# Kernel tuning notes

Measured on AMD Instinct MI355X. Metric: run time of the kernel, lower is better.

The kernel has to match this reference:

```python
import jax, jax.numpy as jnp
import numpy as np

N_NODES = 100000
N_EDGES = 500000
B = 256
NUM_RELS = 200
VEC = 300   # rel_vectors.shape[1]
D = 32      # rel_emb_dim
MODES = 6


def setup_inputs() -> dict:
    key = jax.random.key(0)
    ks = jax.random.split(key, 16)
    s = 0.05
    return {
        'edge_src': jax.random.randint(ks[0], (N_EDGES,), 0, N_NODES, dtype=jnp.int32),
        'edge_dst': jax.random.randint(ks[1], (N_EDGES,), 0, N_NODES, dtype=jnp.int32),
        'edge_type': jax.random.randint(ks[2], (N_EDGES,), 0, NUM_RELS, dtype=jnp.int32),
        'head_ids': jnp.arange(B, dtype=jnp.int32),            # one head node per subgraph
        'tail_ids': jnp.arange(B, dtype=jnp.int32) + B,        # one tail node per subgraph (disjoint)
        'rel_labels': jax.random.randint(ks[3], (B,), 0, NUM_RELS, dtype=jnp.int32),
        'rel_vectors': jax.random.normal(ks[4], (NUM_RELS, VEC), jnp.float32),
        'W1': jax.random.normal(ks[5], (VEC, D), jnp.float32) * s,
        'b1': jax.random.normal(ks[6], (D,), jnp.float32) * s,
        'W2': jax.random.normal(ks[7], (D, D), jnp.float32) * s,
        'b2': jax.random.normal(ks[8], (D,), jnp.float32) * s,
        'reld_W': jax.random.normal(ks[9], (MODES, D, D), jnp.float32) * s,
        'reld_b': jax.random.normal(ks[10], (MODES, D), jnp.float32) * s,
        'conc_W': jax.random.normal(ks[11], (2 * D, D), jnp.float32) * s,
        'conc_b': jax.random.normal(ks[12], (D,), jnp.float32) * s,
        'fc_W': jax.random.normal(ks[13], (D, 1), jnp.float32) * s,
        'fc_b': jax.random.normal(ks[14], (1,), jnp.float32) * s,
    }


def _mode_segments(edge_src, edge_dst, head_ids, tail_ids):
    """Per-edge segment id (batch index, or B=dropped) for each of the 6 modes.
    Equivalent to the torch sparse mask build: mode5 = out_edge_out*in_edge_in,
    mode6 = in_edge_out*out_edge_in, modes 1-4 with overlaps subtracted out."""
    b = head_ids.shape[0]
    bidx = jnp.arange(b, dtype=jnp.int32)
    head_batch = jnp.full((N_NODES,), -1, jnp.int32).at[head_ids].set(bidx)
    tail_batch = jnp.full((N_NODES,), -1, jnp.int32).at[tail_ids].set(bidx)
    hb_s = head_batch[edge_src]
    hb_d = head_batch[edge_dst]
    tb_s = tail_batch[edge_src]
    tb_d = tail_batch[edge_dst]
    m5 = (hb_s >= 0) & (hb_s == tb_d)   # src==head_b and dst==tail_b
    m6 = (hb_d >= 0) & (hb_d == tb_s)   # dst==head_b and src==tail_b
    drop = jnp.int32(b)
    return [
        jnp.where((hb_d >= 0) & ~m6, hb_d, drop),  # in_edge_out  - mode6
        jnp.where((hb_s >= 0) & ~m5, hb_s, drop),  # out_edge_out - mode5
        jnp.where((tb_d >= 0) & ~m5, tb_d, drop),  # in_edge_in   - mode5
        jnp.where((tb_s >= 0) & ~m6, tb_s, drop),  # out_edge_in  - mode6
        jnp.where(m5, hb_s, drop),                 # mode5
        jnp.where(m6, hb_d, drop),                 # mode6
    ]


def reference(edge_src, edge_dst, edge_type, head_ids, tail_ids, rel_labels,
              rel_vectors, W1, b1, W2, b2, reld_W, reld_b, conc_W, conc_b, fc_W, fc_b):
    b = head_ids.shape[0]
    segs = _mode_segments(edge_src, edge_dst, head_ids, tail_ids)

    # edge embeddings: rel_vectors[type] -> transform1 -> transform2   [E, D]
    e = rel_vectors[edge_type] @ W1 + b1
    e = e @ W2 + b2
    # per-mode fc_reld transforms: [MODES, E, D]
    Y = jnp.einsum('ed,mdk->mek', e, reld_W) + reld_b[:, None, :]

    ones_e = jnp.ones(edge_src.shape, e.dtype)
    acc = jnp.zeros((b, Y.shape[-1]), e.dtype)
    for i in range(MODES):
        agg = jax.ops.segment_sum(Y[i], segs[i], num_segments=b + 1)[:b]
        cnt = jax.ops.segment_sum(ones_e, segs[i], num_segments=b + 1)[:b]
        acc = acc + agg / (cnt[:, None] + 1e-30)
    rel_neighbor = acc / MODES

    r = rel_vectors[rel_labels] @ W1 + b1
    r = r @ W2 + b2

    h = jnp.concatenate([rel_neighbor, r], axis=-1) @ conc_W + conc_b
    h = jax.nn.relu(h)
    # F.normalize(p=2, dim=-1)
    g_rep = h / jnp.maximum(jnp.linalg.norm(h, axis=-1, keepdims=True), 1e-12)
    return g_rep @ fc_W + fc_b  # [B, 1]
```

## Files before the change

kernel.cpp:

```cpp
#include <hip/hip_runtime.h>
#include <hip/hip_bf16.h>

constexpr int N_NODES  = 100000;
constexpr int BATCH    = 256;
constexpr int NUM_RELS = 200;
constexpr int VEC      = 300;
constexpr int DIM      = 32;
constexpr int MODES    = 6;

constexpr int BLOCK        = 256;
constexpr int BM_WORDS     = (N_NODES + 31) / 32;
constexpr int RELS_PER_BLK = 8;
constexpr int NRB          = NUM_RELS / RELS_PER_BLK;
static_assert(NUM_RELS % RELS_PER_BLK == 0, "rel blocks assume exact tiling");
constexpr int EDGE_BLKS    = 256;
constexpr int CAP          = 64;
constexpr int HASHN        = 1024;
constexpr unsigned HEMPTY  = 0xFFFFFFFFu;
constexpr int MAXM         = 512;

template <typename T> __device__ __forceinline__ float ldf(const void* p, int i);
template <> __device__ __forceinline__ float ldf<float>(const void* p, int i) {
    return ((const float*)p)[i];
}
template <> __device__ __forceinline__ float ldf<__hip_bfloat16>(const void* p, int i) {
    return __bfloat162float(((const __hip_bfloat16*)p)[i]);
}

__device__ __forceinline__ void detect_dtype(const void* rel_vectors, int* sflag) {
    const int tid = threadIdx.x;
    if (tid < 64) {
        unsigned short p = ((const unsigned short*)rel_vectors)[tid];
        unsigned long long mk = __ballot(((p >> 7) & 0xFF) > 140);
        if (tid == 0) *sflag = (mk == 0ull);
    }
    __syncthreads();
}

__device__ __forceinline__ void hinsert(unsigned* hkey, unsigned* hval, int node, unsigned v) {
    unsigned h = ((unsigned)node * 2654435761u) >> 22;
    for (;;) {
        unsigned prev = atomicCAS(&hkey[h], HEMPTY, (unsigned)node);
        if (prev == HEMPTY || prev == (unsigned)node) { atomicOr(&hval[h], v); return; }
        h = (h + 1) & (HASHN - 1);
    }
}
__device__ __forceinline__ unsigned hlookup(const unsigned* hkey, const unsigned* hval, int node) {
    unsigned h = ((unsigned)node * 2654435761u) >> 22;
    for (;;) {
        const unsigned k = hkey[h];
        if (k == (unsigned)node) return hval[h];
        if (k == HEMPTY) return 0u;
        h = (h + 1) & (HASHN - 1);
    }
}

template <typename T>
__device__ __forceinline__ void rel_body(const void* rel_vectors, const void* W1, const void* b1,
                                         const void* W2, const void* b2,
                                         const void* reld_W, const void* reld_b,
                                         float* E_rel, float* Y_rel,
                                         float (*rv)[VEC], float (*e1)[DIM], float (*e2)[DIM],
                                         int r0) {
    const int tid = threadIdx.x;
    const int g = tid >> 5, d = tid & 31;
    const int r = r0 + g;
    for (int v = d; v < VEC; v += 32) rv[g][v] = ldf<T>(rel_vectors, r * VEC + v);
    __syncthreads();
    float acc = ldf<T>(b1, d);
    for (int v = 0; v < VEC; ++v) acc += rv[g][v] * ldf<T>(W1, v * DIM + d);
    e1[g][d] = acc;
    __syncthreads();
    float a2 = ldf<T>(b2, d);
    for (int k = 0; k < DIM; ++k) a2 += e1[g][k] * ldf<T>(W2, k * DIM + d);
    e2[g][d] = a2;
    E_rel[r * DIM + d] = a2;
    __syncthreads();
    for (int m = 0; m < MODES; ++m) {
        float y = ldf<T>(reld_b, m * DIM + d);
        for (int k = 0; k < DIM; ++k) y += e2[g][k] * ldf<T>(reld_W, (m * DIM + k) * DIM + d);
        Y_rel[(m * NUM_RELS + r) * DIM + d] = y;
    }
}

struct EdgeSmem {
    unsigned bm[BM_WORDS];
    unsigned hkey[HASHN];
    unsigned hval[HASHN];
    unsigned obuf[CAP];
    int ocnt;
};
struct RelSmem {
    float rv[RELS_PER_BLK][VEC];
    float e1[RELS_PER_BLK][DIM];
    float e2[RELS_PER_BLK][DIM];
    int sflag;
};

__global__ __launch_bounds__(BLOCK) void k_main(
        const int* __restrict__ edge_src, const int* __restrict__ edge_dst,
        const int* __restrict__ edge_type,
        const int* __restrict__ head_ids, const int* __restrict__ tail_ids,
        const void* rel_vectors, const void* W1, const void* b1,
        const void* W2, const void* b2, const void* reld_W, const void* reld_b,
        unsigned* list, unsigned* listcnt, float* E_rel, float* Y_rel, int n_edges) {
    union SmemU { RelSmem rel; EdgeSmem edge; };
    __shared__ SmemU s;
    const int bid = blockIdx.x, tid = threadIdx.x;

    if (bid < NRB) {
        detect_dtype(rel_vectors, &s.rel.sflag);
        const int r0 = bid * RELS_PER_BLK;
        if (s.rel.sflag)
            rel_body<__hip_bfloat16>(rel_vectors, W1, b1, W2, b2, reld_W, reld_b,
                                     E_rel, Y_rel, s.rel.rv, s.rel.e1, s.rel.e2, r0);
        else
            rel_body<float>(rel_vectors, W1, b1, W2, b2, reld_W, reld_b,
                            E_rel, Y_rel, s.rel.rv, s.rel.e1, s.rel.e2, r0);
        return;
    }

    const int eb = bid - NRB;
    for (int i = tid; i < BM_WORDS; i += BLOCK) s.edge.bm[i] = 0u;
    for (int i = tid; i < HASHN; i += BLOCK) { s.edge.hkey[i] = HEMPTY; s.edge.hval[i] = 0u; }
    if (tid == 0) s.edge.ocnt = 0;
    __syncthreads();
    if (tid < BATCH) {
        const int h = head_ids[tid], t = tail_ids[tid];
        atomicOr(&s.edge.bm[h >> 5], 1u << (h & 31));
        atomicOr(&s.edge.bm[t >> 5], 1u << (t & 31));
        hinsert(s.edge.hkey, s.edge.hval, h, (unsigned)(tid + 1));
        hinsert(s.edge.hkey, s.edge.hval, t, (unsigned)(tid + 1) << 16);
    }
    __syncthreads();

    auto emit = [&](unsigned code) {
        const int idx = atomicAdd(&s.edge.ocnt, 1);
        if (idx < CAP) s.edge.obuf[idx] = code;
    };
    auto classify = [&](int sn, int dn, unsigned bs, unsigned bd, int e) {
        const int t = edge_type[e];
        const unsigned ps = bs ? hlookup(s.edge.hkey, s.edge.hval, sn) : 0u;
        const unsigned pd = bd ? hlookup(s.edge.hkey, s.edge.hval, dn) : 0u;
        const int hbs = (int)(ps & 0xFFFFu) - 1, tbs = (int)(ps >> 16) - 1;
        const int hbd = (int)(pd & 0xFFFFu) - 1, tbd = (int)(pd >> 16) - 1;
        const bool m5 = (hbs >= 0) && (hbs == tbd);
        const bool m6 = (hbd >= 0) && (hbd == tbs);
        if (hbd >= 0)        emit(((m6 ? 5u : 0u) * BATCH + hbd) * NUM_RELS + t);
        if (hbs >= 0)        emit(((m5 ? 4u : 1u) * BATCH + hbs) * NUM_RELS + t);
        if (tbd >= 0 && !m5) emit((2u * BATCH + tbd) * NUM_RELS + t);
        if (tbs >= 0 && !m6) emit((3u * BATCH + tbs) * NUM_RELS + t);
    };

    const int n4 = n_edges >> 2;
    const int sstr = EDGE_BLKS * BLOCK;
    const int et = eb * BLOCK + tid;
    const int4* src4 = (const int4*)edge_src;
    const int4* dst4 = (const int4*)edge_dst;
    for (int i = et; i < n4; i += sstr) {
        const int4 s4 = src4[i];
        const int4 d4 = dst4[i];
        #pragma unroll
        for (int j = 0; j < 4; ++j) {
            const int sn = (&s4.x)[j];
            const int dn = (&d4.x)[j];
            const unsigned bs = (s.edge.bm[sn >> 5] >> (sn & 31)) & 1u;
            const unsigned bd = (s.edge.bm[dn >> 5] >> (dn & 31)) & 1u;
            if (!(bs | bd)) continue;
            classify(sn, dn, bs, bd, i * 4 + j);
        }
    }
    const int rem = n_edges & 3;
    if (et < rem) {
        const int e = n4 * 4 + et;
        const int sn = edge_src[e], dn = edge_dst[e];
        const unsigned bs = (s.edge.bm[sn >> 5] >> (sn & 31)) & 1u;
        const unsigned bd = (s.edge.bm[dn >> 5] >> (dn & 31)) & 1u;
        if (bs | bd) classify(sn, dn, bs, bd, e);
    }
    __syncthreads();
    const int oc = min(s.edge.ocnt, CAP);
    if (tid == 0) listcnt[eb] = (unsigned)oc;
    for (int i = tid; i < oc; i += BLOCK) list[i * EDGE_BLKS + eb] = s.edge.obuf[i];
}

template <typename T>
__device__ __forceinline__ void epilogue_math(const float* cat,
                                              const void* conc_W, const void* conc_b,
                                              const void* fc_W, const void* fc_b,
                                              void* out, int b) {
    const int tid = threadIdx.x;
    if (tid < DIM) {
        float h = ldf<T>(conc_b, tid);
        for (int k = 0; k < 2 * DIM; ++k) h += cat[k] * ldf<T>(conc_W, k * DIM + tid);
        h = fmaxf(h, 0.f);
        float n2 = h * h;
        #pragma unroll
        for (int off = 16; off >= 1; off >>= 1) n2 += __shfl_xor(n2, off);
        const float g = h / fmaxf(sqrtf(n2), 1e-12f);
        float pr = g * ldf<T>(fc_W, tid);
        #pragma unroll
        for (int off = 16; off >= 1; off >>= 1) pr += __shfl_xor(pr, off);
        if (tid == 0) {
            const float o = pr + ldf<T>(fc_b, 0);
            if constexpr (sizeof(T) == 2) ((__hip_bfloat16*)out)[b] = __float2bfloat16(o);
            else                          ((float*)out)[b] = o;
        }
    }
}

__global__ __launch_bounds__(256) void k_final(
        const unsigned* __restrict__ list, const unsigned* __restrict__ listcnt,
        const float* __restrict__ E_rel, const float* __restrict__ Y_rel,
        const int* __restrict__ rel_labels, const void* rel_vectors,
        const void* conc_W, const void* conc_b, const void* fc_W, const void* fc_b,
        void* out) {
    __shared__ float    accf[MODES][DIM];
    __shared__ float    totf[MODES];
    __shared__ unsigned mbuf[MAXM];
    __shared__ int      mcnt;
    __shared__ float    cat[2 * DIM];
    __shared__ int      sflag;
    const int b = blockIdx.x, tid = threadIdx.x;

    for (int i = tid; i < MODES * DIM; i += 256) ((float*)accf)[i] = 0.f;
    if (tid < MODES) totf[tid] = 0.f;
    if (tid == 0) mcnt = 0;
    const int c = (int)listcnt[tid];
    detect_dtype(rel_vectors, &sflag);

    for (int i = 0; i < c; ++i) {
        const unsigned code = list[i * EDGE_BLKS + tid];
        const int bb = (int)((code / NUM_RELS) % BATCH);
        if (bb == b) {
            const int k = atomicAdd(&mcnt, 1);
            if (k < MAXM) mbuf[k] = code;
        }
    }
    __syncthreads();

    const int mc = min(mcnt, MAXM);
    const int d = tid & 31;
    for (int j = tid >> 5; j < mc; j += 8) {
        const unsigned code = mbuf[j];
        const int m = (int)(code / (NUM_RELS * BATCH));
        const int t = (int)(code % NUM_RELS);
        atomicAdd(&accf[m][d], Y_rel[(m * NUM_RELS + t) * DIM + d]);
        if (d == 0) atomicAdd(&totf[m], 1.f);
    }
    __syncthreads();

    if (tid < DIM) {
        float rn = 0.f;
        for (int m = 0; m < MODES; ++m) rn += accf[m][tid] / (totf[m] + 1e-30f);
        cat[tid] = rn / (float)MODES;
        cat[DIM + tid] = E_rel[rel_labels[b] * DIM + tid];
    }
    __syncthreads();
    if (sflag) epilogue_math<__hip_bfloat16>(cat, conc_W, conc_b, fc_W, fc_b, out, b);
    else       epilogue_math<float>(cat, conc_W, conc_b, fc_W, fc_b, out, b);
}

extern "C" void kernel_launch(void* const* d_in, const int* in_sizes, int n_in,
                              void* d_out, int out_size, void* d_ws, size_t ws_size,
                              hipStream_t stream) {
    const int* edge_src   = (const int*)d_in[0];
    const int* edge_dst   = (const int*)d_in[1];
    const int* edge_type  = (const int*)d_in[2];
    const int* head_ids   = (const int*)d_in[3];
    const int* tail_ids   = (const int*)d_in[4];
    const int* rel_labels = (const int*)d_in[5];
    const void* rel_vectors = d_in[6];
    const void* W1     = d_in[7];
    const void* b1     = d_in[8];
    const void* W2     = d_in[9];
    const void* b2     = d_in[10];
    const void* reld_W = d_in[11];
    const void* reld_b = d_in[12];
    const void* conc_W = d_in[13];
    const void* conc_b = d_in[14];
    const void* fc_W   = d_in[15];
    const void* fc_b   = d_in[16];

    const int n_edges = in_sizes[0];

    unsigned* list    = (unsigned*)d_ws;
    unsigned* listcnt = list + EDGE_BLKS * CAP;
    float*    E_rel   = (float*)(listcnt + EDGE_BLKS);
    float*    Y_rel   = E_rel + NUM_RELS * DIM;

    k_main<<<NRB + EDGE_BLKS, BLOCK, 0, stream>>>(
        edge_src, edge_dst, edge_type, head_ids, tail_ids,
        rel_vectors, W1, b1, W2, b2, reld_W, reld_b,
        list, listcnt, E_rel, Y_rel, n_edges);
    k_final<<<BATCH, 256, 0, stream>>>(
        list, listcnt, E_rel, Y_rel, rel_labels, rel_vectors,
        conc_W, conc_b, fc_W, fc_b, d_out);
}
```

Measured before the change: 116.3 us.

## Fuse main and final kernels with a grid-wide atomic barrier

```diff
diff --git a/kernel.cpp b/kernel.cpp
--- a/kernel.cpp
+++ b/kernel.cpp
@@ -18,6 +18,7 @@
 constexpr int HASHN        = 1024;
 constexpr unsigned HEMPTY  = 0xFFFFFFFFu;
 constexpr int MAXM         = 512;
+constexpr int NPROD        = NRB + EDGE_BLKS;
 
 template <typename T> __device__ __forceinline__ float ldf(const void* p, int i);
 template <> __device__ __forceinline__ float ldf<float>(const void* p, int i) {
@@ -81,107 +82,6 @@
         for (int k = 0; k < DIM; ++k) y += e2[g][k] * ldf<T>(reld_W, (m * DIM + k) * DIM + d);
         Y_rel[(m * NUM_RELS + r) * DIM + d] = y;
     }
-}
-
-struct EdgeSmem {
-    unsigned bm[BM_WORDS];
-    unsigned hkey[HASHN];
-    unsigned hval[HASHN];
-    unsigned obuf[CAP];
-    int ocnt;
-};
-struct RelSmem {
-    float rv[RELS_PER_BLK][VEC];
-    float e1[RELS_PER_BLK][DIM];
-    float e2[RELS_PER_BLK][DIM];
-    int sflag;
-};
-
-__global__ __launch_bounds__(BLOCK) void k_main(
-        const int* __restrict__ edge_src, const int* __restrict__ edge_dst,
-        const int* __restrict__ edge_type,
-        const int* __restrict__ head_ids, const int* __restrict__ tail_ids,
-        const void* rel_vectors, const void* W1, const void* b1,
-        const void* W2, const void* b2, const void* reld_W, const void* reld_b,
-        unsigned* list, unsigned* listcnt, float* E_rel, float* Y_rel, int n_edges) {
-    union SmemU { RelSmem rel; EdgeSmem edge; };
-    __shared__ SmemU s;
-    const int bid = blockIdx.x, tid = threadIdx.x;
-
-    if (bid < NRB) {
-        detect_dtype(rel_vectors, &s.rel.sflag);
-        const int r0 = bid * RELS_PER_BLK;
-        if (s.rel.sflag)
-            rel_body<__hip_bfloat16>(rel_vectors, W1, b1, W2, b2, reld_W, reld_b,
-                                     E_rel, Y_rel, s.rel.rv, s.rel.e1, s.rel.e2, r0);
-        else
-            rel_body<float>(rel_vectors, W1, b1, W2, b2, reld_W, reld_b,
-                            E_rel, Y_rel, s.rel.rv, s.rel.e1, s.rel.e2, r0);
-        return;
-    }
-
-    const int eb = bid - NRB;
-    for (int i = tid; i < BM_WORDS; i += BLOCK) s.edge.bm[i] = 0u;
-    for (int i = tid; i < HASHN; i += BLOCK) { s.edge.hkey[i] = HEMPTY; s.edge.hval[i] = 0u; }
-    if (tid == 0) s.edge.ocnt = 0;
-    __syncthreads();
-    if (tid < BATCH) {
-        const int h = head_ids[tid], t = tail_ids[tid];
-        atomicOr(&s.edge.bm[h >> 5], 1u << (h & 31));
-        atomicOr(&s.edge.bm[t >> 5], 1u << (t & 31));
-        hinsert(s.edge.hkey, s.edge.hval, h, (unsigned)(tid + 1));
-        hinsert(s.edge.hkey, s.edge.hval, t, (unsigned)(tid + 1) << 16);
-    }
-    __syncthreads();
-
-    auto emit = [&](unsigned code) {
-        const int idx = atomicAdd(&s.edge.ocnt, 1);
-        if (idx < CAP) s.edge.obuf[idx] = code;
-    };
-    auto classify = [&](int sn, int dn, unsigned bs, unsigned bd, int e) {
-        const int t = edge_type[e];
-        const unsigned ps = bs ? hlookup(s.edge.hkey, s.edge.hval, sn) : 0u;
-        const unsigned pd = bd ? hlookup(s.edge.hkey, s.edge.hval, dn) : 0u;
-        const int hbs = (int)(ps & 0xFFFFu) - 1, tbs = (int)(ps >> 16) - 1;
-        const int hbd = (int)(pd & 0xFFFFu) - 1, tbd = (int)(pd >> 16) - 1;
-        const bool m5 = (hbs >= 0) && (hbs == tbd);
-        const bool m6 = (hbd >= 0) && (hbd == tbs);
-        if (hbd >= 0)        emit(((m6 ? 5u : 0u) * BATCH + hbd) * NUM_RELS + t);
-        if (hbs >= 0)        emit(((m5 ? 4u : 1u) * BATCH + hbs) * NUM_RELS + t);
-        if (tbd >= 0 && !m5) emit((2u * BATCH + tbd) * NUM_RELS + t);
-        if (tbs >= 0 && !m6) emit((3u * BATCH + tbs) * NUM_RELS + t);
-    };
-
-    const int n4 = n_edges >> 2;
-    const int sstr = EDGE_BLKS * BLOCK;
-    const int et = eb * BLOCK + tid;
-    const int4* src4 = (const int4*)edge_src;
-    const int4* dst4 = (const int4*)edge_dst;
-    for (int i = et; i < n4; i += sstr) {
-        const int4 s4 = src4[i];
-        const int4 d4 = dst4[i];
-        #pragma unroll
-        for (int j = 0; j < 4; ++j) {
-            const int sn = (&s4.x)[j];
-            const int dn = (&d4.x)[j];
-            const unsigned bs = (s.edge.bm[sn >> 5] >> (sn & 31)) & 1u;
-            const unsigned bd = (s.edge.bm[dn >> 5] >> (dn & 31)) & 1u;
-            if (!(bs | bd)) continue;
-            classify(sn, dn, bs, bd, i * 4 + j);
-        }
-    }
-    const int rem = n_edges & 3;
-    if (et < rem) {
-        const int e = n4 * 4 + et;
-        const int sn = edge_src[e], dn = edge_dst[e];
-        const unsigned bs = (s.edge.bm[sn >> 5] >> (sn & 31)) & 1u;
-        const unsigned bd = (s.edge.bm[dn >> 5] >> (dn & 31)) & 1u;
-        if (bs | bd) classify(sn, dn, bs, bd, e);
-    }
-    __syncthreads();
-    const int oc = min(s.edge.ocnt, CAP);
-    if (tid == 0) listcnt[eb] = (unsigned)oc;
-    for (int i = tid; i < oc; i += BLOCK) list[i * EDGE_BLKS + eb] = s.edge.obuf[i];
 }
 
 template <typename T>
@@ -209,56 +109,167 @@
     }
 }
 
-__global__ __launch_bounds__(256) void k_final(
-        const unsigned* __restrict__ list, const unsigned* __restrict__ listcnt,
-        const float* __restrict__ E_rel, const float* __restrict__ Y_rel,
-        const int* __restrict__ rel_labels, const void* rel_vectors,
+struct EdgeSmem {
+    unsigned bm[BM_WORDS];
+    unsigned hkey[HASHN];
+    unsigned hval[HASHN];
+    unsigned obuf[CAP];
+    int ocnt;
+};
+struct RelSmem {
+    float rv[RELS_PER_BLK][VEC];
+    float e1[RELS_PER_BLK][DIM];
+    float e2[RELS_PER_BLK][DIM];
+    int sflag;
+};
+struct FinSmem {
+    float    accf[MODES][DIM];
+    float    totf[MODES];
+    unsigned mbuf[MAXM];
+    int      mcnt;
+    float    cat[2 * DIM];
+    int      sflag;
+};
+
+__global__ __launch_bounds__(BLOCK) void k_fused(
+        const int* __restrict__ edge_src, const int* __restrict__ edge_dst,
+        const int* __restrict__ edge_type,
+        const int* __restrict__ head_ids, const int* __restrict__ tail_ids,
+        const int* __restrict__ rel_labels,
+        const void* rel_vectors, const void* W1, const void* b1,
+        const void* W2, const void* b2, const void* reld_W, const void* reld_b,
         const void* conc_W, const void* conc_b, const void* fc_W, const void* fc_b,
-        void* out) {
-    __shared__ float    accf[MODES][DIM];
-    __shared__ float    totf[MODES];
-    __shared__ unsigned mbuf[MAXM];
-    __shared__ int      mcnt;
-    __shared__ float    cat[2 * DIM];
-    __shared__ int      sflag;
-    const int b = blockIdx.x, tid = threadIdx.x;
-
-    for (int i = tid; i < MODES * DIM; i += 256) ((float*)accf)[i] = 0.f;
-    if (tid < MODES) totf[tid] = 0.f;
-    if (tid == 0) mcnt = 0;
+        unsigned* list, unsigned* listcnt, float* E_rel, float* Y_rel,
+        int* done, void* out, int n_edges) {
+    union SmemU { RelSmem rel; EdgeSmem edge; FinSmem fin; };
+    __shared__ SmemU s;
+    const int bid = blockIdx.x, tid = threadIdx.x;
+
+    if (bid < NRB) {
+        detect_dtype(rel_vectors, &s.rel.sflag);
+        const int r0 = bid * RELS_PER_BLK;
+        if (s.rel.sflag)
+            rel_body<__hip_bfloat16>(rel_vectors, W1, b1, W2, b2, reld_W, reld_b,
+                                     E_rel, Y_rel, s.rel.rv, s.rel.e1, s.rel.e2, r0);
+        else
+            rel_body<float>(rel_vectors, W1, b1, W2, b2, reld_W, reld_b,
+                            E_rel, Y_rel, s.rel.rv, s.rel.e1, s.rel.e2, r0);
+        __threadfence();
+        __syncthreads();
+        if (tid == 0) atomicAdd(done, 1);
+        return;
+    }
+
+    const int eb = bid - NRB;
+    for (int i = tid; i < BM_WORDS; i += BLOCK) s.edge.bm[i] = 0u;
+    for (int i = tid; i < HASHN; i += BLOCK) { s.edge.hkey[i] = HEMPTY; s.edge.hval[i] = 0u; }
+    if (tid == 0) s.edge.ocnt = 0;
+    __syncthreads();
+    if (tid < BATCH) {
+        const int h = head_ids[tid], t = tail_ids[tid];
+        atomicOr(&s.edge.bm[h >> 5], 1u << (h & 31));
+        atomicOr(&s.edge.bm[t >> 5], 1u << (t & 31));
+        hinsert(s.edge.hkey, s.edge.hval, h, (unsigned)(tid + 1));
+        hinsert(s.edge.hkey, s.edge.hval, t, (unsigned)(tid + 1) << 16);
+    }
+    __syncthreads();
+
+    auto emit = [&](unsigned code) {
+        const int idx = atomicAdd(&s.edge.ocnt, 1);
+        if (idx < CAP) s.edge.obuf[idx] = code;
+    };
+    auto classify = [&](int sn, int dn, unsigned bs, unsigned bd, int e) {
+        const int t = edge_type[e];
+        const unsigned ps = bs ? hlookup(s.edge.hkey, s.edge.hval, sn) : 0u;
+        const unsigned pd = bd ? hlookup(s.edge.hkey, s.edge.hval, dn) : 0u;
+        const int hbs = (int)(ps & 0xFFFFu) - 1, tbs = (int)(ps >> 16) - 1;
+        const int hbd = (int)(pd & 0xFFFFu) - 1, tbd = (int)(pd >> 16) - 1;
+        const bool m5 = (hbs >= 0) && (hbs == tbd);
+        const bool m6 = (hbd >= 0) && (hbd == tbs);
+        if (hbd >= 0)        emit(((m6 ? 5u : 0u) * BATCH + hbd) * NUM_RELS + t);
+        if (hbs >= 0)        emit(((m5 ? 4u : 1u) * BATCH + hbs) * NUM_RELS + t);
+        if (tbd >= 0 && !m5) emit((2u * BATCH + tbd) * NUM_RELS + t);
+        if (tbs >= 0 && !m6) emit((3u * BATCH + tbs) * NUM_RELS + t);
+    };
+
+    const int n4 = n_edges >> 2;
+    const int sstr = EDGE_BLKS * BLOCK;
+    const int et = eb * BLOCK + tid;
+    const int4* src4 = (const int4*)edge_src;
+    const int4* dst4 = (const int4*)edge_dst;
+    for (int i = et; i < n4; i += sstr) {
+        const int4 s4 = src4[i];
+        const int4 d4 = dst4[i];
+        #pragma unroll
+        for (int j = 0; j < 4; ++j) {
+            const int sn = (&s4.x)[j];
+            const int dn = (&d4.x)[j];
+            const unsigned bs = (s.edge.bm[sn >> 5] >> (sn & 31)) & 1u;
+            const unsigned bd = (s.edge.bm[dn >> 5] >> (dn & 31)) & 1u;
+            if (!(bs | bd)) continue;
+            classify(sn, dn, bs, bd, i * 4 + j);
+        }
+    }
+    const int rem = n_edges & 3;
+    if (et < rem) {
+        const int e = n4 * 4 + et;
+        const int sn = edge_src[e], dn = edge_dst[e];
+        const unsigned bs = (s.edge.bm[sn >> 5] >> (sn & 31)) & 1u;
+        const unsigned bd = (s.edge.bm[dn >> 5] >> (dn & 31)) & 1u;
+        if (bs | bd) classify(sn, dn, bs, bd, e);
+    }
+    __syncthreads();
+    const int oc = min(s.edge.ocnt, CAP);
+    if (tid == 0) listcnt[eb] = (unsigned)oc;
+    for (int i = tid; i < oc; i += BLOCK) list[i * EDGE_BLKS + eb] = s.edge.obuf[i];
+
+    __threadfence();
+    __syncthreads();
+    if (tid == 0) {
+        atomicAdd(done, 1);
+        while (atomicAdd(done, 0) < NPROD)
+            __builtin_amdgcn_s_sleep(2);
+    }
+    __syncthreads();
+    __threadfence();
+
+    const int b = eb;
+    for (int i = tid; i < MODES * DIM; i += BLOCK) ((float*)s.fin.accf)[i] = 0.f;
+    if (tid < MODES) s.fin.totf[tid] = 0.f;
+    if (tid == 0) s.fin.mcnt = 0;
     const int c = (int)listcnt[tid];
-    detect_dtype(rel_vectors, &sflag);
+    detect_dtype(rel_vectors, &s.fin.sflag);
 
     for (int i = 0; i < c; ++i) {
         const unsigned code = list[i * EDGE_BLKS + tid];
         const int bb = (int)((code / NUM_RELS) % BATCH);
         if (bb == b) {
-            const int k = atomicAdd(&mcnt, 1);
-            if (k < MAXM) mbuf[k] = code;
+            const int k = atomicAdd(&s.fin.mcnt, 1);
+            if (k < MAXM) s.fin.mbuf[k] = code;
         }
     }
     __syncthreads();
 
-    const int mc = min(mcnt, MAXM);
+    const int mc = min(s.fin.mcnt, MAXM);
     const int d = tid & 31;
     for (int j = tid >> 5; j < mc; j += 8) {
-        const unsigned code = mbuf[j];
+        const unsigned code = s.fin.mbuf[j];
         const int m = (int)(code / (NUM_RELS * BATCH));
         const int t = (int)(code % NUM_RELS);
-        atomicAdd(&accf[m][d], Y_rel[(m * NUM_RELS + t) * DIM + d]);
-        if (d == 0) atomicAdd(&totf[m], 1.f);
+        atomicAdd(&s.fin.accf[m][d], Y_rel[(m * NUM_RELS + t) * DIM + d]);
+        if (d == 0) atomicAdd(&s.fin.totf[m], 1.f);
     }
     __syncthreads();
 
     if (tid < DIM) {
         float rn = 0.f;
-        for (int m = 0; m < MODES; ++m) rn += accf[m][tid] / (totf[m] + 1e-30f);
-        cat[tid] = rn / (float)MODES;
-        cat[DIM + tid] = E_rel[rel_labels[b] * DIM + tid];
-    }
-    __syncthreads();
-    if (sflag) epilogue_math<__hip_bfloat16>(cat, conc_W, conc_b, fc_W, fc_b, out, b);
-    else       epilogue_math<float>(cat, conc_W, conc_b, fc_W, fc_b, out, b);
+        for (int m = 0; m < MODES; ++m) rn += s.fin.accf[m][tid] / (s.fin.totf[m] + 1e-30f);
+        s.fin.cat[tid] = rn / (float)MODES;
+        s.fin.cat[DIM + tid] = E_rel[rel_labels[b] * DIM + tid];
+    }
+    __syncthreads();
+    if (s.fin.sflag) epilogue_math<__hip_bfloat16>(s.fin.cat, conc_W, conc_b, fc_W, fc_b, out, b);
+    else             epilogue_math<float>(s.fin.cat, conc_W, conc_b, fc_W, fc_b, out, b);
 }
 
 extern "C" void kernel_launch(void* const* d_in, const int* in_sizes, int n_in,
@@ -288,12 +299,12 @@
     unsigned* listcnt = list + EDGE_BLKS * CAP;
     float*    E_rel   = (float*)(listcnt + EDGE_BLKS);
     float*    Y_rel   = E_rel + NUM_RELS * DIM;
-
-    k_main<<<NRB + EDGE_BLKS, BLOCK, 0, stream>>>(
-        edge_src, edge_dst, edge_type, head_ids, tail_ids,
+    int*      done    = (int*)(Y_rel + MODES * NUM_RELS * DIM);
+
+    hipMemsetAsync(done, 0, sizeof(int), stream);
+    k_fused<<<NRB + EDGE_BLKS, BLOCK, 0, stream>>>(
+        edge_src, edge_dst, edge_type, head_ids, tail_ids, rel_labels,
         rel_vectors, W1, b1, W2, b2, reld_W, reld_b,
-        list, listcnt, E_rel, Y_rel, n_edges);
-    k_final<<<BATCH, 256, 0, stream>>>(
-        list, listcnt, E_rel, Y_rel, rel_labels, rel_vectors,
-        conc_W, conc_b, fc_W, fc_b, d_out);
-}
+        conc_W, conc_b, fc_W, fc_b,
+        list, listcnt, E_rel, Y_rel, done, d_out, n_edges);
+}
```

Result: slower. 162.7 us (+39.9%).

## Bucket matched edges per batch via global atomics instead of per-block lists

Applied to the files above, without the earlier changes.

```diff
diff --git a/kernel.cpp b/kernel.cpp
--- a/kernel.cpp
+++ b/kernel.cpp
@@ -8,16 +8,14 @@
 constexpr int DIM      = 32;
 constexpr int MODES    = 6;
 
-constexpr int BLOCK        = 256;
+constexpr int BLOCK        = 1024;
 constexpr int BM_WORDS     = (N_NODES + 31) / 32;
-constexpr int RELS_PER_BLK = 8;
-constexpr int NRB          = NUM_RELS / RELS_PER_BLK;
-static_assert(NUM_RELS % RELS_PER_BLK == 0, "rel blocks assume exact tiling");
+constexpr int RELS_PER_BLK = 32;
+constexpr int NRB          = (NUM_RELS + RELS_PER_BLK - 1) / RELS_PER_BLK;
 constexpr int EDGE_BLKS    = 256;
-constexpr int CAP          = 64;
 constexpr int HASHN        = 1024;
 constexpr unsigned HEMPTY  = 0xFFFFFFFFu;
-constexpr int MAXM         = 512;
+constexpr int MAXB         = 128;
 
 template <typename T> __device__ __forceinline__ float ldf(const void* p, int i);
 template <> __device__ __forceinline__ float ldf<float>(const void* p, int i) {
@@ -65,7 +63,9 @@
     const int tid = threadIdx.x;
     const int g = tid >> 5, d = tid & 31;
     const int r = r0 + g;
-    for (int v = d; v < VEC; v += 32) rv[g][v] = ldf<T>(rel_vectors, r * VEC + v);
+    const bool live = (r < NUM_RELS);
+    const int rc = live ? r : (NUM_RELS - 1);
+    for (int v = d; v < VEC; v += 32) rv[g][v] = ldf<T>(rel_vectors, rc * VEC + v);
     __syncthreads();
     float acc = ldf<T>(b1, d);
     for (int v = 0; v < VEC; ++v) acc += rv[g][v] * ldf<T>(W1, v * DIM + d);
@@ -74,114 +74,13 @@
     float a2 = ldf<T>(b2, d);
     for (int k = 0; k < DIM; ++k) a2 += e1[g][k] * ldf<T>(W2, k * DIM + d);
     e2[g][d] = a2;
-    E_rel[r * DIM + d] = a2;
+    if (live) E_rel[r * DIM + d] = a2;
     __syncthreads();
     for (int m = 0; m < MODES; ++m) {
         float y = ldf<T>(reld_b, m * DIM + d);
         for (int k = 0; k < DIM; ++k) y += e2[g][k] * ldf<T>(reld_W, (m * DIM + k) * DIM + d);
-        Y_rel[(m * NUM_RELS + r) * DIM + d] = y;
-    }
-}
-
-struct EdgeSmem {
-    unsigned bm[BM_WORDS];
-    unsigned hkey[HASHN];
-    unsigned hval[HASHN];
-    unsigned obuf[CAP];
-    int ocnt;
-};
-struct RelSmem {
-    float rv[RELS_PER_BLK][VEC];
-    float e1[RELS_PER_BLK][DIM];
-    float e2[RELS_PER_BLK][DIM];
-    int sflag;
-};
-
-__global__ __launch_bounds__(BLOCK) void k_main(
-        const int* __restrict__ edge_src, const int* __restrict__ edge_dst,
-        const int* __restrict__ edge_type,
-        const int* __restrict__ head_ids, const int* __restrict__ tail_ids,
-        const void* rel_vectors, const void* W1, const void* b1,
-        const void* W2, const void* b2, const void* reld_W, const void* reld_b,
-        unsigned* list, unsigned* listcnt, float* E_rel, float* Y_rel, int n_edges) {
-    union SmemU { RelSmem rel; EdgeSmem edge; };
-    __shared__ SmemU s;
-    const int bid = blockIdx.x, tid = threadIdx.x;
-
-    if (bid < NRB) {
-        detect_dtype(rel_vectors, &s.rel.sflag);
-        const int r0 = bid * RELS_PER_BLK;
-        if (s.rel.sflag)
-            rel_body<__hip_bfloat16>(rel_vectors, W1, b1, W2, b2, reld_W, reld_b,
-                                     E_rel, Y_rel, s.rel.rv, s.rel.e1, s.rel.e2, r0);
-        else
-            rel_body<float>(rel_vectors, W1, b1, W2, b2, reld_W, reld_b,
-                            E_rel, Y_rel, s.rel.rv, s.rel.e1, s.rel.e2, r0);
-        return;
-    }
-
-    const int eb = bid - NRB;
-    for (int i = tid; i < BM_WORDS; i += BLOCK) s.edge.bm[i] = 0u;
-    for (int i = tid; i < HASHN; i += BLOCK) { s.edge.hkey[i] = HEMPTY; s.edge.hval[i] = 0u; }
-    if (tid == 0) s.edge.ocnt = 0;
-    __syncthreads();
-    if (tid < BATCH) {
-        const int h = head_ids[tid], t = tail_ids[tid];
-        atomicOr(&s.edge.bm[h >> 5], 1u << (h & 31));
-        atomicOr(&s.edge.bm[t >> 5], 1u << (t & 31));
-        hinsert(s.edge.hkey, s.edge.hval, h, (unsigned)(tid + 1));
-        hinsert(s.edge.hkey, s.edge.hval, t, (unsigned)(tid + 1) << 16);
-    }
-    __syncthreads();
-
-    auto emit = [&](unsigned code) {
-        const int idx = atomicAdd(&s.edge.ocnt, 1);
-        if (idx < CAP) s.edge.obuf[idx] = code;
-    };
-    auto classify = [&](int sn, int dn, unsigned bs, unsigned bd, int e) {
-        const int t = edge_type[e];
-        const unsigned ps = bs ? hlookup(s.edge.hkey, s.edge.hval, sn) : 0u;
-        const unsigned pd = bd ? hlookup(s.edge.hkey, s.edge.hval, dn) : 0u;
-        const int hbs = (int)(ps & 0xFFFFu) - 1, tbs = (int)(ps >> 16) - 1;
-        const int hbd = (int)(pd & 0xFFFFu) - 1, tbd = (int)(pd >> 16) - 1;
-        const bool m5 = (hbs >= 0) && (hbs == tbd);
-        const bool m6 = (hbd >= 0) && (hbd == tbs);
-        if (hbd >= 0)        emit(((m6 ? 5u : 0u) * BATCH + hbd) * NUM_RELS + t);
-        if (hbs >= 0)        emit(((m5 ? 4u : 1u) * BATCH + hbs) * NUM_RELS + t);
-        if (tbd >= 0 && !m5) emit((2u * BATCH + tbd) * NUM_RELS + t);
-        if (tbs >= 0 && !m6) emit((3u * BATCH + tbs) * NUM_RELS + t);
-    };
-
-    const int n4 = n_edges >> 2;
-    const int sstr = EDGE_BLKS * BLOCK;
-    const int et = eb * BLOCK + tid;
-    const int4* src4 = (const int4*)edge_src;
-    const int4* dst4 = (const int4*)edge_dst;
-    for (int i = et; i < n4; i += sstr) {
-        const int4 s4 = src4[i];
-        const int4 d4 = dst4[i];
-        #pragma unroll
-        for (int j = 0; j < 4; ++j) {
-            const int sn = (&s4.x)[j];
-            const int dn = (&d4.x)[j];
-            const unsigned bs = (s.edge.bm[sn >> 5] >> (sn & 31)) & 1u;
-            const unsigned bd = (s.edge.bm[dn >> 5] >> (dn & 31)) & 1u;
-            if (!(bs | bd)) continue;
-            classify(sn, dn, bs, bd, i * 4 + j);
-        }
-    }
-    const int rem = n_edges & 3;
-    if (et < rem) {
-        const int e = n4 * 4 + et;
-        const int sn = edge_src[e], dn = edge_dst[e];
-        const unsigned bs = (s.edge.bm[sn >> 5] >> (sn & 31)) & 1u;
-        const unsigned bd = (s.edge.bm[dn >> 5] >> (dn & 31)) & 1u;
-        if (bs | bd) classify(sn, dn, bs, bd, e);
-    }
-    __syncthreads();
-    const int oc = min(s.edge.ocnt, CAP);
-    if (tid == 0) listcnt[eb] = (unsigned)oc;
-    for (int i = tid; i < oc; i += BLOCK) list[i * EDGE_BLKS + eb] = s.edge.obuf[i];
+        if (live) Y_rel[(m * NUM_RELS + r) * DIM + d] = y;
+    }
 }
 
 template <typename T>
@@ -209,41 +108,124 @@
     }
 }
 
+struct EdgeSmem {
+    unsigned bm[BM_WORDS];
+    unsigned hkey[HASHN];
+    unsigned hval[HASHN];
+};
+struct RelSmem {
+    float rv[RELS_PER_BLK][VEC];
+    float e1[RELS_PER_BLK][DIM];
+    float e2[RELS_PER_BLK][DIM];
+    int sflag;
+};
+
+__global__ __launch_bounds__(BLOCK) void k_main(
+        const int* __restrict__ edge_src, const int* __restrict__ edge_dst,
+        const int* __restrict__ edge_type,
+        const int* __restrict__ head_ids, const int* __restrict__ tail_ids,
+        const void* rel_vectors, const void* W1, const void* b1,
+        const void* W2, const void* b2, const void* reld_W, const void* reld_b,
+        unsigned* __restrict__ bucket, unsigned* __restrict__ bcnt,
+        float* __restrict__ E_rel, float* __restrict__ Y_rel, int n_edges) {
+    union SmemU { RelSmem rel; EdgeSmem edge; };
+    __shared__ SmemU s;
+    const int bid = blockIdx.x, tid = threadIdx.x;
+
+    if (bid < NRB) {
+        detect_dtype(rel_vectors, &s.rel.sflag);
+        const int r0 = bid * RELS_PER_BLK;
+        if (s.rel.sflag)
+            rel_body<__hip_bfloat16>(rel_vectors, W1, b1, W2, b2, reld_W, reld_b,
+                                     E_rel, Y_rel, s.rel.rv, s.rel.e1, s.rel.e2, r0);
+        else
+            rel_body<float>(rel_vectors, W1, b1, W2, b2, reld_W, reld_b,
+                            E_rel, Y_rel, s.rel.rv, s.rel.e1, s.rel.e2, r0);
+        return;
+    }
+
+    const int eb = bid - NRB;
+    for (int i = tid; i < BM_WORDS; i += BLOCK) s.edge.bm[i] = 0u;
+    for (int i = tid; i < HASHN; i += BLOCK) { s.edge.hkey[i] = HEMPTY; s.edge.hval[i] = 0u; }
+    __syncthreads();
+    if (tid < BATCH) {
+        const int h = head_ids[tid], t = tail_ids[tid];
+        atomicOr(&s.edge.bm[h >> 5], 1u << (h & 31));
+        atomicOr(&s.edge.bm[t >> 5], 1u << (t & 31));
+        hinsert(s.edge.hkey, s.edge.hval, h, (unsigned)(tid + 1));
+        hinsert(s.edge.hkey, s.edge.hval, t, (unsigned)(tid + 1) << 16);
+    }
+    __syncthreads();
+
+    auto emit = [&](int bb, unsigned code) {
+        const unsigned idx = atomicAdd(&bcnt[bb], 1u);
+        if (idx < (unsigned)MAXB) bucket[bb * MAXB + (int)idx] = code;
+    };
+    auto classify = [&](int sn, int dn, unsigned bs, unsigned bd, int e) {
+        const unsigned t = (unsigned)edge_type[e];
+        const unsigned ps = bs ? hlookup(s.edge.hkey, s.edge.hval, sn) : 0u;
+        const unsigned pd = bd ? hlookup(s.edge.hkey, s.edge.hval, dn) : 0u;
+        const int hbs = (int)(ps & 0xFFFFu) - 1, tbs = (int)(ps >> 16) - 1;
+        const int hbd = (int)(pd & 0xFFFFu) - 1, tbd = (int)(pd >> 16) - 1;
+        const bool m5 = (hbs >= 0) && (hbs == tbd);
+        const bool m6 = (hbd >= 0) && (hbd == tbs);
+        if (hbd >= 0)        emit(hbd, (m6 ? 5u : 0u) * NUM_RELS + t);
+        if (hbs >= 0)        emit(hbs, (m5 ? 4u : 1u) * NUM_RELS + t);
+        if (tbd >= 0 && !m5) emit(tbd, 2u * NUM_RELS + t);
+        if (tbs >= 0 && !m6) emit(tbs, 3u * NUM_RELS + t);
+    };
+
+    const int n4 = n_edges >> 2;
+    const int sstr = EDGE_BLKS * BLOCK;
+    const int et = eb * BLOCK + tid;
+    const int4* src4 = (const int4*)edge_src;
+    const int4* dst4 = (const int4*)edge_dst;
+    for (int i = et; i < n4; i += sstr) {
+        const int4 s4 = src4[i];
+        const int4 d4 = dst4[i];
+        #pragma unroll
+        for (int j = 0; j < 4; ++j) {
+            const int sn = (&s4.x)[j];
+            const int dn = (&d4.x)[j];
+            const unsigned bs = (s.edge.bm[sn >> 5] >> (sn & 31)) & 1u;
+            const unsigned bd = (s.edge.bm[dn >> 5] >> (dn & 31)) & 1u;
+            if (!(bs | bd)) continue;
+            classify(sn, dn, bs, bd, i * 4 + j);
+        }
+    }
+    const int rem = n_edges & 3;
+    if (et < rem) {
+        const int e = n4 * 4 + et;
+        const int sn = edge_src[e], dn = edge_dst[e];
+        const unsigned bs = (s.edge.bm[sn >> 5] >> (sn & 31)) & 1u;
+        const unsigned bd = (s.edge.bm[dn >> 5] >> (dn & 31)) & 1u;
+        if (bs | bd) classify(sn, dn, bs, bd, e);
+    }
+}
+
 __global__ __launch_bounds__(256) void k_final(
-        const unsigned* __restrict__ list, const unsigned* __restrict__ listcnt,
+        const unsigned* __restrict__ bucket, const unsigned* __restrict__ bcnt,
         const float* __restrict__ E_rel, const float* __restrict__ Y_rel,
         const int* __restrict__ rel_labels, const void* rel_vectors,
         const void* conc_W, const void* conc_b, const void* fc_W, const void* fc_b,
         void* out) {
     __shared__ float    accf[MODES][DIM];
     __shared__ float    totf[MODES];
-    __shared__ unsigned mbuf[MAXM];
-    __shared__ int      mcnt;
+    __shared__ unsigned mbuf[MAXB];
     __shared__ float    cat[2 * DIM];
     __shared__ int      sflag;
     const int b = blockIdx.x, tid = threadIdx.x;
 
     for (int i = tid; i < MODES * DIM; i += 256) ((float*)accf)[i] = 0.f;
     if (tid < MODES) totf[tid] = 0.f;
-    if (tid == 0) mcnt = 0;
-    const int c = (int)listcnt[tid];
+    const int mc = min((int)bcnt[b], MAXB);
+    if (tid < mc) mbuf[tid] = bucket[b * MAXB + tid];
     detect_dtype(rel_vectors, &sflag);
 
-    for (int i = 0; i < c; ++i) {
-        const unsigned code = list[i * EDGE_BLKS + tid];
-        const int bb = (int)((code / NUM_RELS) % BATCH);
-        if (bb == b) {
-            const int k = atomicAdd(&mcnt, 1);
-            if (k < MAXM) mbuf[k] = code;
-        }
-    }
-    __syncthreads();
-
-    const int mc = min(mcnt, MAXM);
     const int d = tid & 31;
     for (int j = tid >> 5; j < mc; j += 8) {
         const unsigned code = mbuf[j];
-        const int m = (int)(code / (NUM_RELS * BATCH));
+        const int m = (int)(code / NUM_RELS);
         const int t = (int)(code % NUM_RELS);
         atomicAdd(&accf[m][d], Y_rel[(m * NUM_RELS + t) * DIM + d]);
         if (d == 0) atomicAdd(&totf[m], 1.f);
@@ -284,16 +266,17 @@
 
     const int n_edges = in_sizes[0];
 
-    unsigned* list    = (unsigned*)d_ws;
-    unsigned* listcnt = list + EDGE_BLKS * CAP;
-    float*    E_rel   = (float*)(listcnt + EDGE_BLKS);
-    float*    Y_rel   = E_rel + NUM_RELS * DIM;
-
+    unsigned* bucket = (unsigned*)d_ws;
+    unsigned* bcnt   = bucket + BATCH * MAXB;
+    float*    E_rel  = (float*)(bcnt + BATCH);
+    float*    Y_rel  = E_rel + NUM_RELS * DIM;
+
+    hipMemsetAsync(bcnt, 0, BATCH * sizeof(unsigned), stream);
     k_main<<<NRB + EDGE_BLKS, BLOCK, 0, stream>>>(
         edge_src, edge_dst, edge_type, head_ids, tail_ids,
         rel_vectors, W1, b1, W2, b2, reld_W, reld_b,
-        list, listcnt, E_rel, Y_rel, n_edges);
+        bucket, bcnt, E_rel, Y_rel, n_edges);
     k_final<<<BATCH, 256, 0, stream>>>(
-        list, listcnt, E_rel, Y_rel, rel_labels, rel_vectors,
+        bucket, bcnt, E_rel, Y_rel, rel_labels, rel_vectors,
         conc_W, conc_b, fc_W, fc_b, d_out);
 }
```

Result: no change. 114.3 us (-1.7%).

## Enlarge blocks to 1024 threads and skip idle edge blocks

Applied to the files above, without the earlier changes.

```diff
diff --git a/kernel.cpp b/kernel.cpp
--- a/kernel.cpp
+++ b/kernel.cpp
@@ -8,15 +8,14 @@
 constexpr int DIM      = 32;
 constexpr int MODES    = 6;
 
-constexpr int BLOCK        = 256;
+constexpr int BLOCK        = 1024;
 constexpr int BM_WORDS     = (N_NODES + 31) / 32;
-constexpr int RELS_PER_BLK = 8;
-constexpr int NRB          = NUM_RELS / RELS_PER_BLK;
-static_assert(NUM_RELS % RELS_PER_BLK == 0, "rel blocks assume exact tiling");
+constexpr int RELS_PER_BLK = 32;
+constexpr int NRB          = (NUM_RELS + RELS_PER_BLK - 1) / RELS_PER_BLK;
 constexpr int EDGE_BLKS    = 256;
-constexpr int CAP          = 64;
 constexpr int HASHN        = 1024;
 constexpr unsigned HEMPTY  = 0xFFFFFFFFu;
+constexpr int CAP          = 128;
 constexpr int MAXM         = 512;
 
 template <typename T> __device__ __forceinline__ float ldf(const void* p, int i);
@@ -65,7 +64,9 @@
     const int tid = threadIdx.x;
     const int g = tid >> 5, d = tid & 31;
     const int r = r0 + g;
-    for (int v = d; v < VEC; v += 32) rv[g][v] = ldf<T>(rel_vectors, r * VEC + v);
+    const bool live = (r < NUM_RELS);
+    const int rc = live ? r : (NUM_RELS - 1);
+    for (int v = d; v < VEC; v += 32) rv[g][v] = ldf<T>(rel_vectors, rc * VEC + v);
     __syncthreads();
     float acc = ldf<T>(b1, d);
     for (int v = 0; v < VEC; ++v) acc += rv[g][v] * ldf<T>(W1, v * DIM + d);
@@ -74,114 +75,13 @@
     float a2 = ldf<T>(b2, d);
     for (int k = 0; k < DIM; ++k) a2 += e1[g][k] * ldf<T>(W2, k * DIM + d);
     e2[g][d] = a2;
-    E_rel[r * DIM + d] = a2;
+    if (live) E_rel[r * DIM + d] = a2;
     __syncthreads();
     for (int m = 0; m < MODES; ++m) {
         float y = ldf<T>(reld_b, m * DIM + d);
         for (int k = 0; k < DIM; ++k) y += e2[g][k] * ldf<T>(reld_W, (m * DIM + k) * DIM + d);
-        Y_rel[(m * NUM_RELS + r) * DIM + d] = y;
-    }
-}
-
-struct EdgeSmem {
-    unsigned bm[BM_WORDS];
-    unsigned hkey[HASHN];
-    unsigned hval[HASHN];
-    unsigned obuf[CAP];
-    int ocnt;
-};
-struct RelSmem {
-    float rv[RELS_PER_BLK][VEC];
-    float e1[RELS_PER_BLK][DIM];
-    float e2[RELS_PER_BLK][DIM];
-    int sflag;
-};
-
-__global__ __launch_bounds__(BLOCK) void k_main(
-        const int* __restrict__ edge_src, const int* __restrict__ edge_dst,
-        const int* __restrict__ edge_type,
-        const int* __restrict__ head_ids, const int* __restrict__ tail_ids,
-        const void* rel_vectors, const void* W1, const void* b1,
-        const void* W2, const void* b2, const void* reld_W, const void* reld_b,
-        unsigned* list, unsigned* listcnt, float* E_rel, float* Y_rel, int n_edges) {
-    union SmemU { RelSmem rel; EdgeSmem edge; };
-    __shared__ SmemU s;
-    const int bid = blockIdx.x, tid = threadIdx.x;
-
-    if (bid < NRB) {
-        detect_dtype(rel_vectors, &s.rel.sflag);
-        const int r0 = bid * RELS_PER_BLK;
-        if (s.rel.sflag)
-            rel_body<__hip_bfloat16>(rel_vectors, W1, b1, W2, b2, reld_W, reld_b,
-                                     E_rel, Y_rel, s.rel.rv, s.rel.e1, s.rel.e2, r0);
-        else
-            rel_body<float>(rel_vectors, W1, b1, W2, b2, reld_W, reld_b,
-                            E_rel, Y_rel, s.rel.rv, s.rel.e1, s.rel.e2, r0);
-        return;
-    }
-
-    const int eb = bid - NRB;
-    for (int i = tid; i < BM_WORDS; i += BLOCK) s.edge.bm[i] = 0u;
-    for (int i = tid; i < HASHN; i += BLOCK) { s.edge.hkey[i] = HEMPTY; s.edge.hval[i] = 0u; }
-    if (tid == 0) s.edge.ocnt = 0;
-    __syncthreads();
-    if (tid < BATCH) {
-        const int h = head_ids[tid], t = tail_ids[tid];
-        atomicOr(&s.edge.bm[h >> 5], 1u << (h & 31));
-        atomicOr(&s.edge.bm[t >> 5], 1u << (t & 31));
-        hinsert(s.edge.hkey, s.edge.hval, h, (unsigned)(tid + 1));
-        hinsert(s.edge.hkey, s.edge.hval, t, (unsigned)(tid + 1) << 16);
-    }
-    __syncthreads();
-
-    auto emit = [&](unsigned code) {
-        const int idx = atomicAdd(&s.edge.ocnt, 1);
-        if (idx < CAP) s.edge.obuf[idx] = code;
-    };
-    auto classify = [&](int sn, int dn, unsigned bs, unsigned bd, int e) {
-        const int t = edge_type[e];
-        const unsigned ps = bs ? hlookup(s.edge.hkey, s.edge.hval, sn) : 0u;
-        const unsigned pd = bd ? hlookup(s.edge.hkey, s.edge.hval, dn) : 0u;
-        const int hbs = (int)(ps & 0xFFFFu) - 1, tbs = (int)(ps >> 16) - 1;
-        const int hbd = (int)(pd & 0xFFFFu) - 1, tbd = (int)(pd >> 16) - 1;
-        const bool m5 = (hbs >= 0) && (hbs == tbd);
-        const bool m6 = (hbd >= 0) && (hbd == tbs);
-        if (hbd >= 0)        emit(((m6 ? 5u : 0u) * BATCH + hbd) * NUM_RELS + t);
-        if (hbs >= 0)        emit(((m5 ? 4u : 1u) * BATCH + hbs) * NUM_RELS + t);
-        if (tbd >= 0 && !m5) emit((2u * BATCH + tbd) * NUM_RELS + t);
-        if (tbs >= 0 && !m6) emit((3u * BATCH + tbs) * NUM_RELS + t);
-    };
-
-    const int n4 = n_edges >> 2;
-    const int sstr = EDGE_BLKS * BLOCK;
-    const int et = eb * BLOCK + tid;
-    const int4* src4 = (const int4*)edge_src;
-    const int4* dst4 = (const int4*)edge_dst;
-    for (int i = et; i < n4; i += sstr) {
-        const int4 s4 = src4[i];
-        const int4 d4 = dst4[i];
-        #pragma unroll
-        for (int j = 0; j < 4; ++j) {
-            const int sn = (&s4.x)[j];
-            const int dn = (&d4.x)[j];
-            const unsigned bs = (s.edge.bm[sn >> 5] >> (sn & 31)) & 1u;
-            const unsigned bd = (s.edge.bm[dn >> 5] >> (dn & 31)) & 1u;
-            if (!(bs | bd)) continue;
-            classify(sn, dn, bs, bd, i * 4 + j);
-        }
-    }
-    const int rem = n_edges & 3;
-    if (et < rem) {
-        const int e = n4 * 4 + et;
-        const int sn = edge_src[e], dn = edge_dst[e];
-        const unsigned bs = (s.edge.bm[sn >> 5] >> (sn & 31)) & 1u;
-        const unsigned bd = (s.edge.bm[dn >> 5] >> (dn & 31)) & 1u;
-        if (bs | bd) classify(sn, dn, bs, bd, e);
-    }
-    __syncthreads();
-    const int oc = min(s.edge.ocnt, CAP);
-    if (tid == 0) listcnt[eb] = (unsigned)oc;
-    for (int i = tid; i < oc; i += BLOCK) list[i * EDGE_BLKS + eb] = s.edge.obuf[i];
+        if (live) Y_rel[(m * NUM_RELS + r) * DIM + d] = y;
+    }
 }
 
 template <typename T>
@@ -209,7 +109,114 @@
     }
 }
 
-__global__ __launch_bounds__(256) void k_final(
+struct EdgeSmem {
+    unsigned bm[BM_WORDS];
+    unsigned hkey[HASHN];
+    unsigned hval[HASHN];
+    unsigned obuf[CAP];
+    int ocnt;
+};
+struct RelSmem {
+    float rv[RELS_PER_BLK][VEC];
+    float e1[RELS_PER_BLK][DIM];
+    float e2[RELS_PER_BLK][DIM];
+    int sflag;
+};
+
+__global__ __launch_bounds__(BLOCK) void k_main(
+        const int* __restrict__ edge_src, const int* __restrict__ edge_dst,
+        const int* __restrict__ edge_type,
+        const int* __restrict__ head_ids, const int* __restrict__ tail_ids,
+        const void* rel_vectors, const void* W1, const void* b1,
+        const void* W2, const void* b2, const void* reld_W, const void* reld_b,
+        unsigned* __restrict__ list, unsigned* __restrict__ listcnt,
+        float* __restrict__ E_rel, float* __restrict__ Y_rel, int n_edges) {
+    union SmemU { RelSmem rel; EdgeSmem edge; };
+    __shared__ SmemU s;
+    const int bid = blockIdx.x, tid = threadIdx.x;
+
+    if (bid < NRB) {
+        detect_dtype(rel_vectors, &s.rel.sflag);
+        const int r0 = bid * RELS_PER_BLK;
+        if (s.rel.sflag)
+            rel_body<__hip_bfloat16>(rel_vectors, W1, b1, W2, b2, reld_W, reld_b,
+                                     E_rel, Y_rel, s.rel.rv, s.rel.e1, s.rel.e2, r0);
+        else
+            rel_body<float>(rel_vectors, W1, b1, W2, b2, reld_W, reld_b,
+                            E_rel, Y_rel, s.rel.rv, s.rel.e1, s.rel.e2, r0);
+        return;
+    }
+
+    const int eb = bid - NRB;
+    const int n4c = (n_edges + 3) >> 2;
+    if (eb * BLOCK >= n4c) {
+        if (tid == 0) listcnt[eb] = 0u;
+        return;
+    }
+    for (int i = tid; i < BM_WORDS; i += BLOCK) s.edge.bm[i] = 0u;
+    for (int i = tid; i < HASHN; i += BLOCK) { s.edge.hkey[i] = HEMPTY; s.edge.hval[i] = 0u; }
+    if (tid == 0) s.edge.ocnt = 0;
+    __syncthreads();
+    if (tid < BATCH) {
+        const int h = head_ids[tid], t = tail_ids[tid];
+        atomicOr(&s.edge.bm[h >> 5], 1u << (h & 31));
+        atomicOr(&s.edge.bm[t >> 5], 1u << (t & 31));
+        hinsert(s.edge.hkey, s.edge.hval, h, (unsigned)(tid + 1));
+        hinsert(s.edge.hkey, s.edge.hval, t, (unsigned)(tid + 1) << 16);
+    }
+    __syncthreads();
+
+    auto emit = [&](unsigned code) {
+        const int idx = atomicAdd(&s.edge.ocnt, 1);
+        if (idx < CAP) s.edge.obuf[idx] = code;
+    };
+    auto classify = [&](int sn, int dn, unsigned bs, unsigned bd, int e) {
+        const unsigned t = (unsigned)edge_type[e];
+        const unsigned ps = bs ? hlookup(s.edge.hkey, s.edge.hval, sn) : 0u;
+        const unsigned pd = bd ? hlookup(s.edge.hkey, s.edge.hval, dn) : 0u;
+        const int hbs = (int)(ps & 0xFFFFu) - 1, tbs = (int)(ps >> 16) - 1;
+        const int hbd = (int)(pd & 0xFFFFu) - 1, tbd = (int)(pd >> 16) - 1;
+        const bool m5 = (hbs >= 0) && (hbs == tbd);
+        const bool m6 = (hbd >= 0) && (hbd == tbs);
+        if (hbd >= 0)        emit(((m6 ? 5u : 0u) * BATCH + (unsigned)hbd) * NUM_RELS + t);
+        if (hbs >= 0)        emit(((m5 ? 4u : 1u) * BATCH + (unsigned)hbs) * NUM_RELS + t);
+        if (tbd >= 0 && !m5) emit((2u * BATCH + (unsigned)tbd) * NUM_RELS + t);
+        if (tbs >= 0 && !m6) emit((3u * BATCH + (unsigned)tbs) * NUM_RELS + t);
+    };
+
+    const int n4 = n_edges >> 2;
+    const int sstr = EDGE_BLKS * BLOCK;
+    const int et = eb * BLOCK + tid;
+    const int4* src4 = (const int4*)edge_src;
+    const int4* dst4 = (const int4*)edge_dst;
+    for (int i = et; i < n4; i += sstr) {
+        const int4 s4 = src4[i];
+        const int4 d4 = dst4[i];
+        #pragma unroll
+        for (int j = 0; j < 4; ++j) {
+            const int sn = (&s4.x)[j];
+            const int dn = (&d4.x)[j];
+            const unsigned bs = (s.edge.bm[sn >> 5] >> (sn & 31)) & 1u;
+            const unsigned bd = (s.edge.bm[dn >> 5] >> (dn & 31)) & 1u;
+            if (!(bs | bd)) continue;
+            classify(sn, dn, bs, bd, i * 4 + j);
+        }
+    }
+    const int rem = n_edges & 3;
+    if (et < rem) {
+        const int e = n4 * 4 + et;
+        const int sn = edge_src[e], dn = edge_dst[e];
+        const unsigned bs = (s.edge.bm[sn >> 5] >> (sn & 31)) & 1u;
+        const unsigned bd = (s.edge.bm[dn >> 5] >> (dn & 31)) & 1u;
+        if (bs | bd) classify(sn, dn, bs, bd, e);
+    }
+    __syncthreads();
+    const int oc = min(s.edge.ocnt, CAP);
+    if (tid == 0) listcnt[eb] = (unsigned)oc;
+    for (int i = tid; i < oc; i += BLOCK) list[i * EDGE_BLKS + eb] = s.edge.obuf[i];
+}
+
+__global__ __launch_bounds__(BLOCK) void k_final(
         const unsigned* __restrict__ list, const unsigned* __restrict__ listcnt,
         const float* __restrict__ E_rel, const float* __restrict__ Y_rel,
         const int* __restrict__ rel_labels, const void* rel_vectors,
@@ -223,14 +230,16 @@
     __shared__ int      sflag;
     const int b = blockIdx.x, tid = threadIdx.x;
 
-    for (int i = tid; i < MODES * DIM; i += 256) ((float*)accf)[i] = 0.f;
+    for (int i = tid; i < MODES * DIM; i += BLOCK) ((float*)accf)[i] = 0.f;
     if (tid < MODES) totf[tid] = 0.f;
     if (tid == 0) mcnt = 0;
-    const int c = (int)listcnt[tid];
+    const int seg = tid & (EDGE_BLKS - 1);
+    const int r0  = tid >> 8;
+    const int c   = (int)listcnt[seg];
     detect_dtype(rel_vectors, &sflag);
 
-    for (int i = 0; i < c; ++i) {
-        const unsigned code = list[i * EDGE_BLKS + tid];
+    for (int i = r0; i < c; i += 4) {
+        const unsigned code = list[i * EDGE_BLKS + seg];
         const int bb = (int)((code / NUM_RELS) % BATCH);
         if (bb == b) {
             const int k = atomicAdd(&mcnt, 1);
@@ -241,7 +250,7 @@
 
     const int mc = min(mcnt, MAXM);
     const int d = tid & 31;
-    for (int j = tid >> 5; j < mc; j += 8) {
+    for (int j = tid >> 5; j < mc; j += BLOCK / 32) {
         const unsigned code = mbuf[j];
         const int m = (int)(code / (NUM_RELS * BATCH));
         const int t = (int)(code % NUM_RELS);
@@ -293,7 +302,7 @@
         edge_src, edge_dst, edge_type, head_ids, tail_ids,
         rel_vectors, W1, b1, W2, b2, reld_W, reld_b,
         list, listcnt, E_rel, Y_rel, n_edges);
-    k_final<<<BATCH, 256, 0, stream>>>(
+    k_final<<<BATCH, BLOCK, 0, stream>>>(
         list, listcnt, E_rel, Y_rel, rel_labels, rel_vectors,
         conc_W, conc_b, fc_W, fc_b, d_out);
 }
```

Result: no change. 114.6 us (-1.5%).
